# Optimization experiments

Hardware: AMD Instinct MI355X
Metric: run time of the kernel (lower is better)

Reference implementation:

```python
import jax, jax.numpy as jnp
import numpy as np

B, N, C, H = 128, 197, 768, 12
D = C // H
SCALE = D ** -0.5


def setup_inputs() -> dict:
    key = jax.random.key(0)
    k1, k2, k3, k4 = jax.random.split(key, 4)
    x = jax.random.normal(k1, (B, N, C), dtype=jnp.float32)
    qkv_w = jax.random.normal(k2, (3 * C, C), dtype=jnp.float32) * 0.02
    proj_w = jax.random.normal(k3, (C, C), dtype=jnp.float32) * 0.02
    proj_b = jax.random.normal(k4, (C,), dtype=jnp.float32) * 0.02
    pi_init = 1.0 / (197.0 ** 0.25)
    pi_q = jnp.full((1, H, N, 1), pi_init, dtype=jnp.float32)
    pi_k = jnp.full((1, H, 1, N), pi_init, dtype=jnp.float32)
    return {"x": x, "qkv_w": qkv_w, "proj_w": proj_w, "proj_b": proj_b,
            "pi_q": pi_q, "pi_k": pi_k}


def reference(x, qkv_w, proj_w, proj_b, pi_q, pi_k):
    b, n, c = x.shape
    qkv = (x @ qkv_w.T).reshape(b, n, 3, H, D).transpose(2, 0, 3, 1, 4)
    q, k, v = qkv[0], qkv[1], qkv[2]
    # pairwise squared distance ||q_i - k_j||^2 via GEMM form
    q2 = jnp.sum(q * q, axis=-1)                      # [B,H,N]
    k2 = jnp.sum(k * k, axis=-1)                      # [B,H,N]
    qk = jnp.einsum('bhnd,bhmd->bhnm', q, k)          # [B,H,N,N]
    sq = jnp.maximum(q2[..., :, None] + k2[..., None, :] - 2.0 * qk, 0.0)
    attn = jnp.exp(-SCALE / 2.0 * sq)                 # [B,H,N,N]
    # qk_pi weighting: clamp(|pi_q|,max=1) * clamp(|pi_k|,max=1)
    pi = jnp.minimum(jnp.abs(pi_q), 1.0) * jnp.minimum(jnp.abs(pi_k), 1.0)
    attn = attn * pi
    attn = attn / (jnp.sum(attn, axis=-1, keepdims=True) + 1e-6)
    out = jnp.einsum('bhnm,bhmd->bhnd', attn, v)      # [B,H,N,D]
    out = out.transpose(0, 2, 1, 3).reshape(b, n, c)
    return out @ proj_w.T + proj_b
```

## Files before the change

kernel.cpp:

```cpp
#include <hip/hip_runtime.h>

typedef __attribute__((ext_vector_type(8))) short bf16x8;
typedef __attribute__((ext_vector_type(8))) unsigned short u16x8;
typedef __attribute__((ext_vector_type(4))) float f32x4;

#define MFMA16(a, b, c) __builtin_amdgcn_mfma_f32_16x16x32_bf16((a), (b), (c), 0, 0, 0)

__device__ __forceinline__ unsigned short f2bf(float f) {
  union { float f; unsigned u; } x; x.f = f;
  unsigned r = x.u + 0x7FFFu + ((x.u >> 16) & 1u);
  return (unsigned short)(r >> 16);
}
__device__ __forceinline__ float bf2f(unsigned short b) {
  union { unsigned u; float f; } x; x.u = ((unsigned)b) << 16;
  return x.f;
}

__device__ __forceinline__ void gld_lds16(const void* g, void* l) {
  __builtin_amdgcn_global_load_lds(
      (const __attribute__((address_space(1))) unsigned int*)g,
      (__attribute__((address_space(3))) unsigned int*)l, 16, 0, 0);
}

__global__ __launch_bounds__(256) void cvt3_kernel(const float* __restrict__ s0,
                                                   unsigned short* __restrict__ d0, int n0,
                                                   const float* __restrict__ s1,
                                                   unsigned short* __restrict__ d1, int n1,
                                                   const float* __restrict__ s2,
                                                   unsigned short* __restrict__ d2, int n2) {
  int i = blockIdx.x * 256 + threadIdx.x;
  const int stride = gridDim.x * 256;
  const int tot = n0 + n1 + n2;
  for (; i < tot; i += stride) {
    const float* s;
    unsigned short* d;
    int j = i;
    if (j < n0) { s = s0; d = d0; }
    else if (j < n0 + n1) { j -= n0; s = s1; d = d1; }
    else { j -= n0 + n1; s = s2; d = d2; }
    float4 f0 = ((const float4*)s)[2 * j];
    float4 f1 = ((const float4*)s)[2 * j + 1];
    u16x8 v;
    v[0] = f2bf(f0.x); v[1] = f2bf(f0.y); v[2] = f2bf(f0.z); v[3] = f2bf(f0.w);
    v[4] = f2bf(f1.x); v[5] = f2bf(f1.y); v[6] = f2bf(f1.z); v[7] = f2bf(f1.w);
    ((u16x8*)d)[j] = v;
  }
}

__global__ __launch_bounds__(256) void qkv_gemm(const unsigned short* __restrict__ X,
                                                const unsigned short* __restrict__ W,
                                                unsigned short* __restrict__ Qo,
                                                unsigned short* __restrict__ Ko,
                                                unsigned short* __restrict__ Vo) {
  __shared__ unsigned short As[128][64];
  __shared__ unsigned short Bs[128][64];
  const int tid = threadIdx.x;
  const int lane = tid & 63, wave = tid >> 6;
  const int lrow = lane & 15, lgrp = lane >> 4;
  const int wr = wave >> 1, wc = wave & 1;
  const int m0 = blockIdx.x * 128, n0 = blockIdx.y * 128;

  f32x4 acc[4][4];
#pragma unroll
  for (int i = 0; i < 4; i++)
#pragma unroll
    for (int j = 0; j < 4; j++) acc[i][j] = (f32x4){0.f, 0.f, 0.f, 0.f};

  const int rbase = wave * 32;
  const int srow = rbase + (lane >> 3);
  const int scol = (lane & 7) * 8;

  for (int k0 = 0; k0 < 768; k0 += 64) {
    const unsigned short* ga = X + (size_t)(m0 + srow) * 768 + k0 + scol;
    const unsigned short* gb = W + (size_t)(n0 + srow) * 768 + k0 + scol;
#pragma unroll
    for (int i = 0; i < 4; i++) {
      gld_lds16(ga + (size_t)i * 8 * 768, &As[rbase + i * 8][0]);
      gld_lds16(gb + (size_t)i * 8 * 768, &Bs[rbase + i * 8][0]);
    }
    __syncthreads();
#pragma unroll
    for (int kk = 0; kk < 2; kk++) {
      bf16x8 a[4], b[4];
#pragma unroll
      for (int f = 0; f < 4; f++) {
        a[f] = *(const bf16x8*)(&As[wr * 64 + f * 16 + lrow][kk * 32 + lgrp * 8]);
        b[f] = *(const bf16x8*)(&Bs[wc * 64 + f * 16 + lrow][kk * 32 + lgrp * 8]);
      }
#pragma unroll
      for (int i = 0; i < 4; i++)
#pragma unroll
        for (int j = 0; j < 4; j++) acc[i][j] = MFMA16(a[i], b[j], acc[i][j]);
    }
    __syncthreads();
  }

#pragma unroll
  for (int fj = 0; fj < 4; fj++) {
    const int jb = n0 + wc * 64 + fj * 16;
    const int s = jb / 768;
    const int hh = (jb % 768) >> 6;
    const int dd = (jb & 63) + lrow;
    unsigned short* dst = (s == 0) ? Qo : (s == 1) ? Ko : Vo;
#pragma unroll
    for (int fi = 0; fi < 4; fi++) {
#pragma unroll
      for (int r = 0; r < 4; r++) {
        int m = m0 + wr * 64 + fi * 16 + lgrp * 4 + r;
        int bb = m / 197;
        int nn = m - bb * 197;
        dst[(size_t)((bb * 12 + hh) * 197 + nn) * 64 + dd] = f2bf(acc[fi][fj][r]);
      }
    }
  }
}

__global__ __launch_bounds__(256) void proj_gemm(const unsigned short* __restrict__ A,
                                                 const unsigned short* __restrict__ W,
                                                 const float* __restrict__ bias,
                                                 float* __restrict__ out) {
  __shared__ unsigned short As[128][64];
  __shared__ unsigned short Bs[128][64];
  const int tid = threadIdx.x;
  const int lane = tid & 63, wave = tid >> 6;
  const int lrow = lane & 15, lgrp = lane >> 4;
  const int wr = wave >> 1, wc = wave & 1;
  const int m0 = blockIdx.x * 128, n0 = blockIdx.y * 128;

  f32x4 acc[4][4];
#pragma unroll
  for (int i = 0; i < 4; i++)
#pragma unroll
    for (int j = 0; j < 4; j++) acc[i][j] = (f32x4){0.f, 0.f, 0.f, 0.f};

  const int rbase = wave * 32;
  const int srow = rbase + (lane >> 3);
  const int scol = (lane & 7) * 8;

  for (int k0 = 0; k0 < 768; k0 += 64) {
    const unsigned short* ga = A + (size_t)(m0 + srow) * 768 + k0 + scol;
    const unsigned short* gb = W + (size_t)(n0 + srow) * 768 + k0 + scol;
#pragma unroll
    for (int i = 0; i < 4; i++) {
      gld_lds16(ga + (size_t)i * 8 * 768, &As[rbase + i * 8][0]);
      gld_lds16(gb + (size_t)i * 8 * 768, &Bs[rbase + i * 8][0]);
    }
    __syncthreads();
#pragma unroll
    for (int kk = 0; kk < 2; kk++) {
      bf16x8 a[4], b[4];
#pragma unroll
      for (int f = 0; f < 4; f++) {
        a[f] = *(const bf16x8*)(&As[wr * 64 + f * 16 + lrow][kk * 32 + lgrp * 8]);
        b[f] = *(const bf16x8*)(&Bs[wc * 64 + f * 16 + lrow][kk * 32 + lgrp * 8]);
      }
#pragma unroll
      for (int i = 0; i < 4; i++)
#pragma unroll
        for (int j = 0; j < 4; j++) acc[i][j] = MFMA16(a[i], b[j], acc[i][j]);
    }
    __syncthreads();
  }

#pragma unroll
  for (int fj = 0; fj < 4; fj++) {
    const int j = n0 + wc * 64 + fj * 16 + lrow;
    const float bj = bias[j];
#pragma unroll
    for (int fi = 0; fi < 4; fi++) {
#pragma unroll
      for (int r = 0; r < 4; r++) {
        int m = m0 + wr * 64 + fi * 16 + lgrp * 4 + r;
        out[(size_t)m * 768 + j] = acc[fi][fj][r] + bj;
      }
    }
  }
}

__global__ __launch_bounds__(512, 4) void attn_kernel(const unsigned short* __restrict__ Q,
                                                      const unsigned short* __restrict__ K,
                                                      const unsigned short* __restrict__ V,
                                                      const float* __restrict__ piq,
                                                      const float* __restrict__ pik,
                                                      unsigned short* __restrict__ Oa) {
  __shared__ __align__(16) unsigned char smem[80896];
  unsigned short* Ks = (unsigned short*)smem;
  unsigned short* Vt = (unsigned short*)(smem + 26624);
  unsigned short* Ps = (unsigned short*)(smem + 54272);
  float* k2c = (float*)(smem + 67072);
  float* lpk = k2c + 208;
  float* piqs = lpk + 208;
  unsigned short* Vlin = (unsigned short*)(smem + 54272);

  const int tid = threadIdx.x;
  const int lane = tid & 63, wave = tid >> 6;
  const int lrow = lane & 15, lgrp = lane >> 4;
  const int bh = blockIdx.x;
  const int h = bh % 12;
  const int b = bh / 12;
  const size_t kvbase = (size_t)bh * 197 * 64;
  const float c1 = -0.09016844005556021f;

  float my_pik = 0.f, my_piq = 0.f;
  if (tid < 197) { my_pik = pik[h * 197 + tid]; my_piq = piq[h * 197 + tid]; }
  const int t0 = wave, t1 = wave + 8;
  const int rq0 = min(t0 * 16 + lrow, 196);
  const int rq1 = (t1 < 13) ? min(t1 * 16 + lrow, 196) : rq0;
  const size_t qb0 = kvbase + (size_t)rq0 * 64 + lgrp * 8;
  const size_t qb1 = kvbase + (size_t)rq1 * 64 + lgrp * 8;
  const bf16x8 aqA0 = *(const bf16x8*)(Q + qb0);
  const bf16x8 aqA1 = *(const bf16x8*)(Q + qb0 + 32);
  const bf16x8 aqB0 = *(const bf16x8*)(Q + qb1);
  const bf16x8 aqB1 = *(const bf16x8*)(Q + qb1 + 32);

  {
    const int rl = lane >> 3;
    const int csw = ((lane & 7) ^ rl) * 8;
    const int cl = (lane & 7) * 8;
    for (int i = wave; i < 26; i += 8) {
      gld_lds16(K + kvbase + (size_t)(i * 8 + rl) * 64 + csw, Ks + i * 512);
      gld_lds16(V + kvbase + (size_t)(i * 8 + rl) * 64 + cl, Vlin + i * 512);
    }
  }
  __syncthreads();

  for (int c = tid; c < 1664; c += 512) {
    const int row = c >> 3, d0 = (c & 7) * 8;
    u16x8 v = *(const u16x8*)(Vlin + row * 64 + d0);
#pragma unroll
    for (int e = 0; e < 8; e++) Vt[(d0 + e) * 216 + row] = (unsigned short)v[e];
  }
  Vt[(tid >> 3) * 216 + 208 + (tid & 7)] = 0;
  __syncthreads();

  if (tid < 208) {
    const int n = tid;
    if (n < 197) {
      float k2 = 0.f;
#pragma unroll
      for (int c = 0; c < 8; c++) {
        u16x8 v = *(const u16x8*)(Ks + n * 64 + ((c ^ (n & 7)) << 3));
#pragma unroll
        for (int e = 0; e < 8; e++) { float f = bf2f((unsigned short)v[e]); k2 += f * f; }
      }
      const float pk = fminf(fabsf(my_pik), 1.f);
      const float lp = log2f(pk);
      lpk[n] = lp;
      k2c[n] = c1 * k2 + lp;
      piqs[n] = fminf(fabsf(my_piq), 1.f);
    } else {
      const float ninf = -__builtin_inff();
      lpk[n] = ninf; k2c[n] = ninf; piqs[n] = 0.f;
    }
  }
  __syncthreads();

  unsigned short* Pw = Ps + wave * 640;

#define ATTN_TILE(TT, AQ0, AQ1)                                               \
  {                                                                           \
    const int n0 = (TT) * 16;                                                 \
    float q2p = 0.f;                                                          \
    _Pragma("unroll") for (int e = 0; e < 8; e++) {                           \
      float f0 = bf2f((unsigned short)((u16x8)(AQ0))[e]); q2p += f0 * f0;     \
      float f1 = bf2f((unsigned short)((u16x8)(AQ1))[e]); q2p += f1 * f1;     \
    }                                                                         \
    q2p += __shfl_xor(q2p, 16);                                               \
    q2p += __shfl_xor(q2p, 32);                                               \
    float q2r[4];                                                             \
    _Pragma("unroll") for (int r = 0; r < 4; r++)                             \
        q2r[r] = __shfl(q2p, lgrp * 4 + r);                                   \
    float rs[4] = {0.f, 0.f, 0.f, 0.f};                                       \
    f32x4 o[4];                                                               \
    _Pragma("unroll") for (int dt = 0; dt < 4; dt++)                          \
        o[dt] = (f32x4){0.f, 0.f, 0.f, 0.f};                                  \
    for (int ks = 0; ks < 7; ks++) {                                          \
      _Pragma("unroll") for (int half = 0; half < 2; half++) {                \
        const int jt = ks * 2 + half;                                         \
        if (jt < 13) {                                                        \
          f32x4 sacc = (f32x4){0.f, 0.f, 0.f, 0.f};                           \
          const int rk = jt * 16 + lrow;                                      \
          bf16x8 bk0 = *(const bf16x8*)(Ks + rk * 64 +                        \
                                        (((0 + lgrp) ^ (rk & 7)) << 3));      \
          bf16x8 bk1 = *(const bf16x8*)(Ks + rk * 64 +                        \
                                        (((4 + lgrp) ^ (rk & 7)) << 3));      \
          sacc = MFMA16((AQ0), bk0, sacc);                                    \
          sacc = MFMA16((AQ1), bk1, sacc);                                    \
          const int j = jt * 16 + lrow;                                       \
          const float k2cj = k2c[j];                                          \
          const float lpkj = lpk[j];                                          \
          _Pragma("unroll") for (int r = 0; r < 4; r++) {                     \
            float t1v = fmaf(-2.f, sacc[r], q2r[r]);                          \
            float arg = fminf(fmaf(c1, t1v, k2cj), lpkj);                     \
            float p = exp2f(arg);                                             \
            rs[r] += p;                                                       \
            Pw[(lgrp * 4 + r) * 40 + half * 16 + lrow] = f2bf(p);             \
          }                                                                   \
        } else {                                                              \
          _Pragma("unroll") for (int r = 0; r < 4; r++)                       \
              Pw[(lgrp * 4 + r) * 40 + 16 + lrow] = 0;                        \
        }                                                                     \
      }                                                                       \
      bf16x8 ap = *(const bf16x8*)(Pw + lrow * 40 + lgrp * 8);                \
      const int jcol = min(ks * 32 + lgrp * 8, 208);                          \
      __builtin_amdgcn_s_setprio(1);                                          \
      _Pragma("unroll") for (int dt = 0; dt < 4; dt++) {                      \
        bf16x8 bv = *(const bf16x8*)(Vt + (dt * 16 + lrow) * 216 + jcol);     \
        o[dt] = MFMA16(ap, bv, o[dt]);                                        \
      }                                                                       \
      __builtin_amdgcn_s_setprio(0);                                          \
    }                                                                         \
    _Pragma("unroll") for (int r = 0; r < 4; r++) {                           \
      float v = rs[r];                                                        \
      v += __shfl_xor(v, 1);                                                  \
      v += __shfl_xor(v, 2);                                                  \
      v += __shfl_xor(v, 4);                                                  \
      v += __shfl_xor(v, 8);                                                  \
      rs[r] = v;                                                              \
    }                                                                         \
    float scale[4];                                                           \
    _Pragma("unroll") for (int r = 0; r < 4; r++) {                           \
      float pq = piqs[n0 + lgrp * 4 + r];                                     \
      scale[r] = pq / (pq * rs[r] + 1e-6f);                                   \
    }                                                                         \
    _Pragma("unroll") for (int r = 0; r < 4; r++) {                           \
      const int n = n0 + lgrp * 4 + r;                                        \
      if (n < 197) {                                                          \
        const size_t ob = ((size_t)(b * 197 + n)) * 768 + h * 64;             \
        _Pragma("unroll") for (int dt = 0; dt < 4; dt++)                      \
            Oa[ob + dt * 16 + lrow] = f2bf(o[dt][r] * scale[r]);              \
      }                                                                       \
    }                                                                         \
  }

  ATTN_TILE(t0, aqA0, aqA1);
  if (t1 < 13) ATTN_TILE(t1, aqB0, aqB1);
#undef ATTN_TILE
}

extern "C" void kernel_launch(void* const* d_in, const int* in_sizes, int n_in,
                              void* d_out, int out_size, void* d_ws, size_t ws_size,
                              hipStream_t stream) {
  const float* x = (const float*)d_in[0];
  const float* qkv_w = (const float*)d_in[1];
  const float* proj_w = (const float*)d_in[2];
  const float* proj_b = (const float*)d_in[3];
  const float* pi_q = (const float*)d_in[4];
  const float* pi_k = (const float*)d_in[5];
  float* out = (float*)d_out;

  unsigned short* ws = (unsigned short*)d_ws;
  const size_t S = (size_t)1536 * 197 * 64;
  unsigned short* Q = ws;
  unsigned short* K = ws + S;
  unsigned short* V = ws + 2 * S;
  unsigned short* Xb = ws + 3 * S;
  unsigned short* Oa = Xb;
  unsigned short* Wb = ws + 4 * S;
  unsigned short* Pb = Wb + (size_t)2304 * 768;

  dim3 blk(256, 1, 1);
  dim3 blk512(512, 1, 1);
  cvt3_kernel<<<dim3(2048, 1, 1), blk, 0, stream>>>(x, Xb, 2420736,
                                                    qkv_w, Wb, 221184,
                                                    proj_w, Pb, 73728);
  qkv_gemm<<<dim3(197, 18, 1), blk, 0, stream>>>(Xb, Wb, Q, K, V);
  attn_kernel<<<dim3(1536, 1, 1), blk512, 0, stream>>>(Q, K, V, pi_q, pi_k, Oa);
  proj_gemm<<<dim3(197, 6, 1), blk, 0, stream>>>(Oa, Pb, proj_b, out);
}
```

Measured before the change: 301.6 us.

## Rewrite QKV and projection GEMMs with 256x256 tiles and multi-stage async pipeline

Both GEMM kernels move from 128x128 tiles on 256 threads to 256x256 tiles on 512 threads, with 8x4 MFMA accumulators per wave. Global-to-LDS staging now uses direct LDS loads issued several K-steps ahead into double-buffered, XOR-swizzled LDS. The loop is paced by explicit vmcnt/lgkmcnt waits, raw s_barrier calls and sched_barriers so that loads overlap MFMA work and LDS bank conflicts drop. The cost is much larger LDS use per block, at most one block per CU, and coarse grids (notably 297 blocks for the projection) that can leave a tail. Padded rows beyond M are still read from the workspace but their stores are masked.

```diff
diff --git a/kernel.cpp b/kernel.cpp
--- a/kernel.cpp
+++ b/kernel.cpp
@@ -47,131 +47,149 @@
   }
 }
 
-__global__ __launch_bounds__(256) void qkv_gemm(const unsigned short* __restrict__ X,
-                                                const unsigned short* __restrict__ W,
-                                                unsigned short* __restrict__ Qo,
-                                                unsigned short* __restrict__ Ko,
-                                                unsigned short* __restrict__ Vo) {
-  __shared__ unsigned short As[128][64];
-  __shared__ unsigned short Bs[128][64];
-  const int tid = threadIdx.x;
-  const int lane = tid & 63, wave = tid >> 6;
-  const int lrow = lane & 15, lgrp = lane >> 4;
-  const int wr = wave >> 1, wc = wave & 1;
-  const int m0 = blockIdx.x * 128, n0 = blockIdx.y * 128;
-
-  f32x4 acc[4][4];
-#pragma unroll
-  for (int i = 0; i < 4; i++)
-#pragma unroll
-    for (int j = 0; j < 4; j++) acc[i][j] = (f32x4){0.f, 0.f, 0.f, 0.f};
-
-  const int rbase = wave * 32;
-  const int srow = rbase + (lane >> 3);
-  const int scol = (lane & 7) * 8;
-
-  for (int k0 = 0; k0 < 768; k0 += 64) {
-    const unsigned short* ga = X + (size_t)(m0 + srow) * 768 + k0 + scol;
-    const unsigned short* gb = W + (size_t)(n0 + srow) * 768 + k0 + scol;
-#pragma unroll
-    for (int i = 0; i < 4; i++) {
-      gld_lds16(ga + (size_t)i * 8 * 768, &As[rbase + i * 8][0]);
-      gld_lds16(gb + (size_t)i * 8 * 768, &Bs[rbase + i * 8][0]);
-    }
-    __syncthreads();
-#pragma unroll
-    for (int kk = 0; kk < 2; kk++) {
-      bf16x8 a[4], b[4];
-#pragma unroll
-      for (int f = 0; f < 4; f++) {
-        a[f] = *(const bf16x8*)(&As[wr * 64 + f * 16 + lrow][kk * 32 + lgrp * 8]);
-        b[f] = *(const bf16x8*)(&Bs[wc * 64 + f * 16 + lrow][kk * 32 + lgrp * 8]);
-      }
-#pragma unroll
-      for (int i = 0; i < 4; i++)
-#pragma unroll
-        for (int j = 0; j < 4; j++) acc[i][j] = MFMA16(a[i], b[j], acc[i][j]);
-    }
-    __syncthreads();
-  }
-
-#pragma unroll
-  for (int fj = 0; fj < 4; fj++) {
-    const int jb = n0 + wc * 64 + fj * 16;
+
+#define G8_PREAMBLE()                                                        \
+  const int tid = threadIdx.x;                                               \
+  const int lane = tid & 63, wave = tid >> 6;                                \
+  const int lrow = lane & 15, lgrp = lane >> 4;                              \
+  const int wr = wave >> 2, wc = wave & 3;                                   \
+  const int m0 = blockIdx.x * 256, n0 = blockIdx.y * 256;                    \
+  f32x4 acc[8][4];                                                           \
+  _Pragma("unroll") for (int i = 0; i < 8; i++)                              \
+      _Pragma("unroll") for (int j = 0; j < 4; j++)                          \
+          acc[i][j] = (f32x4){0.f, 0.f, 0.f, 0.f};                           \
+  const int srow_off = wave * 16 + (lane >> 2);                              \
+  const int scol_off = 8 * ((lane & 3) ^ ((lane >> 2) & 3));
+
+#define STG_HT8(kk)                                                          \
+  {                                                                          \
+    const int q_ = ((kk) >> 2) & 1, t_ = (kk) >> 2;                          \
+    const int tb_ = (kk) & 1, kh_ = ((kk) >> 1) & 1;                         \
+    const unsigned short* s_ = tb_ ? Bsrc : Asrc;                            \
+    const int rb_ = tb_ ? n0 : m0;                                           \
+    unsigned short* d_ =                                                     \
+        (tb_ ? Bbuf : Abuf) + q_ * 16384 + kh_ * 8192 + wave * 512;          \
+    const size_t c_ = (size_t)t_ * 64 + kh_ * 32 + scol_off;                 \
+    gld_lds16(s_ + (size_t)(rb_ + srow_off) * 768 + c_, d_);                 \
+    gld_lds16(s_ + (size_t)(rb_ + srow_off + 128) * 768 + c_, d_ + 4096);    \
+  }
+
+#define SB() __builtin_amdgcn_sched_barrier(0)
+
+#define PHASE8(T, PP)                                                        \
+  {                                                                          \
+    const int q = (T) & 1;                                                   \
+    const int kh = (PP) >> 1, ch = (PP) & 1;                                 \
+    const unsigned short* Ab = Abuf + q * 16384 + kh * 8192;                 \
+    const unsigned short* Bb = Bbuf + q * 16384 + kh * 8192;                 \
+    bf16x8 afr[4];                                                           \
+    _Pragma("unroll") for (int mi = 0; mi < 4; mi++) {                       \
+      const int ra = wr * 128 + ch * 64 + mi * 16 + lrow;                    \
+      afr[mi] = *(const bf16x8*)(Ab + ra * 32 + 8 * (lgrp ^ (lrow & 3)));    \
+    }                                                                        \
+    if (ch == 0) {                                                           \
+      _Pragma("unroll") for (int nf = 0; nf < 4; nf++) {                     \
+        const int rb = wc * 64 + nf * 16 + lrow;                             \
+        bfr[nf] = *(const bf16x8*)(Bb + rb * 32 + 8 * (lgrp ^ (lrow & 3)));  \
+      }                                                                      \
+    }                                                                        \
+    const int ks = 4 * (T) + (PP) + 6;                                       \
+    if (ks < 48) STG_HT8(ks);                                                \
+    SB();                                                                    \
+    __builtin_amdgcn_s_barrier();                                            \
+    asm volatile("s_waitcnt lgkmcnt(0)" ::: "memory");                       \
+    SB();                                                                    \
+    __builtin_amdgcn_s_setprio(1);                                           \
+    _Pragma("unroll") for (int mi = 0; mi < 4; mi++)                         \
+        _Pragma("unroll") for (int nf = 0; nf < 4; nf++)                     \
+            acc[ch * 4 + mi][nf] = MFMA16(afr[mi], bfr[nf],                  \
+                                          acc[ch * 4 + mi][nf]);             \
+    __builtin_amdgcn_s_setprio(0);                                           \
+    if ((PP) == 3) {                                                         \
+      SB();                                                                  \
+      if ((T) < 10)                                                          \
+        asm volatile("s_waitcnt vmcnt(4)" ::: "memory");                     \
+      else if ((T) == 10)                                                    \
+        asm volatile("s_waitcnt vmcnt(0)" ::: "memory");                     \
+    }                                                                        \
+    SB();                                                                    \
+    __builtin_amdgcn_s_barrier();                                            \
+    SB();                                                                    \
+  }
+
+#define G8_MAIN()                                                            \
+  STG_HT8(0); STG_HT8(1); STG_HT8(2); STG_HT8(3); STG_HT8(4); STG_HT8(5);    \
+  SB();                                                                      \
+  asm volatile("s_waitcnt vmcnt(4)" ::: "memory");                           \
+  SB();                                                                      \
+  __builtin_amdgcn_s_barrier();                                              \
+  SB();                                                                      \
+  bf16x8 bfr[4];                                                             \
+  for (int T = 0; T < 12; ++T) {                                             \
+    PHASE8(T, 0);                                                            \
+    PHASE8(T, 1);                                                            \
+    PHASE8(T, 2);                                                            \
+    PHASE8(T, 3);                                                            \
+  }
+
+__global__ __launch_bounds__(512, 2) void qkv_gemm(const unsigned short* __restrict__ Asrc,
+                                                   const unsigned short* __restrict__ Bsrc,
+                                                   unsigned short* __restrict__ Qo,
+                                                   unsigned short* __restrict__ Ko,
+                                                   unsigned short* __restrict__ Vo) {
+  __shared__ unsigned short Abuf[32768];
+  __shared__ unsigned short Bbuf[32768];
+  G8_PREAMBLE();
+  G8_MAIN();
+
+#pragma unroll
+  for (int nf = 0; nf < 4; nf++) {
+    const int jb = n0 + wc * 64 + nf * 16;
     const int s = jb / 768;
     const int hh = (jb % 768) >> 6;
     const int dd = (jb & 63) + lrow;
     unsigned short* dst = (s == 0) ? Qo : (s == 1) ? Ko : Vo;
 #pragma unroll
-    for (int fi = 0; fi < 4; fi++) {
-#pragma unroll
-      for (int r = 0; r < 4; r++) {
-        int m = m0 + wr * 64 + fi * 16 + lgrp * 4 + r;
-        int bb = m / 197;
-        int nn = m - bb * 197;
-        dst[(size_t)((bb * 12 + hh) * 197 + nn) * 64 + dd] = f2bf(acc[fi][fj][r]);
+    for (int ch = 0; ch < 2; ch++) {
+#pragma unroll
+      for (int mi = 0; mi < 4; mi++) {
+#pragma unroll
+        for (int r = 0; r < 4; r++) {
+          const int m = m0 + wr * 128 + ch * 64 + mi * 16 + lgrp * 4 + r;
+          if (m < 25216) {
+            const int bb = m / 197;
+            const int nn = m - bb * 197;
+            dst[(size_t)((bb * 12 + hh) * 197 + nn) * 64 + dd] =
+                f2bf(acc[ch * 4 + mi][nf][r]);
+          }
+        }
       }
     }
   }
 }
 
-__global__ __launch_bounds__(256) void proj_gemm(const unsigned short* __restrict__ A,
-                                                 const unsigned short* __restrict__ W,
-                                                 const float* __restrict__ bias,
-                                                 float* __restrict__ out) {
-  __shared__ unsigned short As[128][64];
-  __shared__ unsigned short Bs[128][64];
-  const int tid = threadIdx.x;
-  const int lane = tid & 63, wave = tid >> 6;
-  const int lrow = lane & 15, lgrp = lane >> 4;
-  const int wr = wave >> 1, wc = wave & 1;
-  const int m0 = blockIdx.x * 128, n0 = blockIdx.y * 128;
-
-  f32x4 acc[4][4];
-#pragma unroll
-  for (int i = 0; i < 4; i++)
-#pragma unroll
-    for (int j = 0; j < 4; j++) acc[i][j] = (f32x4){0.f, 0.f, 0.f, 0.f};
-
-  const int rbase = wave * 32;
-  const int srow = rbase + (lane >> 3);
-  const int scol = (lane & 7) * 8;
-
-  for (int k0 = 0; k0 < 768; k0 += 64) {
-    const unsigned short* ga = A + (size_t)(m0 + srow) * 768 + k0 + scol;
-    const unsigned short* gb = W + (size_t)(n0 + srow) * 768 + k0 + scol;
-#pragma unroll
-    for (int i = 0; i < 4; i++) {
-      gld_lds16(ga + (size_t)i * 8 * 768, &As[rbase + i * 8][0]);
-      gld_lds16(gb + (size_t)i * 8 * 768, &Bs[rbase + i * 8][0]);
-    }
-    __syncthreads();
-#pragma unroll
-    for (int kk = 0; kk < 2; kk++) {
-      bf16x8 a[4], b[4];
-#pragma unroll
-      for (int f = 0; f < 4; f++) {
-        a[f] = *(const bf16x8*)(&As[wr * 64 + f * 16 + lrow][kk * 32 + lgrp * 8]);
-        b[f] = *(const bf16x8*)(&Bs[wc * 64 + f * 16 + lrow][kk * 32 + lgrp * 8]);
-      }
-#pragma unroll
-      for (int i = 0; i < 4; i++)
-#pragma unroll
-        for (int j = 0; j < 4; j++) acc[i][j] = MFMA16(a[i], b[j], acc[i][j]);
-    }
-    __syncthreads();
-  }
-
-#pragma unroll
-  for (int fj = 0; fj < 4; fj++) {
-    const int j = n0 + wc * 64 + fj * 16 + lrow;
+__global__ __launch_bounds__(512, 2) void proj_gemm(const unsigned short* __restrict__ Asrc,
+                                                    const unsigned short* __restrict__ Bsrc,
+                                                    const float* __restrict__ bias,
+                                                    float* __restrict__ out) {
+  __shared__ unsigned short Abuf[32768];
+  __shared__ unsigned short Bbuf[32768];
+  G8_PREAMBLE();
+  G8_MAIN();
+
+#pragma unroll
+  for (int nf = 0; nf < 4; nf++) {
+    const int j = n0 + wc * 64 + nf * 16 + lrow;
     const float bj = bias[j];
 #pragma unroll
-    for (int fi = 0; fi < 4; fi++) {
-#pragma unroll
-      for (int r = 0; r < 4; r++) {
-        int m = m0 + wr * 64 + fi * 16 + lgrp * 4 + r;
-        out[(size_t)m * 768 + j] = acc[fi][fj][r] + bj;
+    for (int ch = 0; ch < 2; ch++) {
+#pragma unroll
+      for (int mi = 0; mi < 4; mi++) {
+#pragma unroll
+        for (int r = 0; r < 4; r++) {
+          const int m = m0 + wr * 128 + ch * 64 + mi * 16 + lgrp * 4 + r;
+          if (m < 25216) out[(size_t)m * 768 + j] = acc[ch * 4 + mi][nf][r] + bj;
+        }
       }
     }
   }
@@ -259,7 +277,7 @@
 
 #define ATTN_TILE(TT, AQ0, AQ1)                                               \
   {                                                                           \
-    const int n0 = (TT) * 16;                                                 \
+    const int n0_ = (TT) * 16;                                                \
     float q2p = 0.f;                                                          \
     _Pragma("unroll") for (int e = 0; e < 8; e++) {                           \
       float f0 = bf2f((unsigned short)((u16x8)(AQ0))[e]); q2p += f0 * f0;     \
@@ -320,11 +338,11 @@
     }                                                                         \
     float scale[4];                                                           \
     _Pragma("unroll") for (int r = 0; r < 4; r++) {                           \
-      float pq = piqs[n0 + lgrp * 4 + r];                                     \
+      float pq = piqs[n0_ + lgrp * 4 + r];                                    \
       scale[r] = pq / (pq * rs[r] + 1e-6f);                                   \
     }                                                                         \
     _Pragma("unroll") for (int r = 0; r < 4; r++) {                           \
-      const int n = n0 + lgrp * 4 + r;                                        \
+      const int n = n0_ + lgrp * 4 + r;                                       \
       if (n < 197) {                                                          \
         const size_t ob = ((size_t)(b * 197 + n)) * 768 + h * 64;             \
         _Pragma("unroll") for (int dt = 0; dt < 4; dt++)                      \
@@ -364,7 +382,7 @@
   cvt3_kernel<<<dim3(2048, 1, 1), blk, 0, stream>>>(x, Xb, 2420736,
                                                     qkv_w, Wb, 221184,
                                                     proj_w, Pb, 73728);
-  qkv_gemm<<<dim3(197, 18, 1), blk, 0, stream>>>(Xb, Wb, Q, K, V);
+  qkv_gemm<<<dim3(99, 9, 1), blk512, 0, stream>>>(Xb, Wb, Q, K, V);
   attn_kernel<<<dim3(1536, 1, 1), blk512, 0, stream>>>(Q, K, V, pi_q, pi_k, Oa);
-  proj_gemm<<<dim3(197, 6, 1), blk, 0, stream>>>(Oa, Pb, proj_b, out);
-}
+  proj_gemm<<<dim3(99, 3, 1), blk512, 0, stream>>>(Oa, Pb, proj_b, out);
+}
```

New measurement: 354.2 us. +17.5%, slower.
